# Kernel tuning notes

Measured on AMD Instinct MI355X. Metric: run time of the kernel, lower is better.

## Reference

```python
import jax, jax.numpy as jnp
import numpy as np

B, D, H0, H1, O = 4096, 1024, 1024, 1024, 1024  # O = output_dim + 1
ALPHA = 0.3
CLAMP = 0.3


def setup_inputs() -> dict:
    key = jax.random.key(0)
    ks = jax.random.split(key, 15)
    def he(k, fan_in, shape):
        return jax.random.normal(k, shape, dtype=jnp.float32) * np.sqrt(2.0 / fan_in).astype(np.float32)
    def heb(k, shape):
        return jax.random.uniform(k, shape, dtype=jnp.float32, minval=-CLAMP, maxval=CLAMP)
    return {
        "x": jax.random.normal(ks[0], (B, D), dtype=jnp.float32),
        "x2h0": he(ks[1], D, (D, H0)),
        "x2h1": he(ks[2], D, (D, H1)),
        "h02h1": he(ks[3], H0, (H0, H1)),
        "x2y": he(ks[4], D, (D, O)),
        "h02y": he(ks[5], H0, (H0, O)),
        "h12y": he(ks[6], H1, (H1, O)),
        "heb_x2h0": heb(ks[7], (D, H0)),
        "heb_x2h1": heb(ks[8], (D, H1)),
        "heb_h02h1": heb(ks[9], (H0, H1)),
        "heb_x2y": heb(ks[10], (D, O)),
        "heb_h02y": heb(ks[11], (H0, O)),
        "heb_h12y": heb(ks[12], (H1, O)),
        "W": jax.random.uniform(ks[13], (1, 1), dtype=jnp.float32),
    }


def reference(x, x2h0, x2h1, h02h1, x2y, h02y, h12y,
              heb_x2h0, heb_x2h1, heb_h02h1, heb_x2y, heb_h02y, heb_h12y, W):
    clamp = lambda m: jnp.clip(m, -CLAMP, CLAMP)
    # x -> h0
    h0_x = x @ (x2h0 + W * heb_x2h0)                       # [B, H0]
    heb_x2h0_n = clamp(heb_x2h0 + ALPHA * (x.T @ h0_x))
    h0 = jax.nn.relu(h0_x)
    # x -> h1, h0 -> h1
    h1_x = x @ (x2h1 + W * heb_x2h1)                       # [B, H1]
    heb_x2h1_n = clamp(heb_x2h1 + ALPHA * (x.T @ h1_x))
    h1_0 = h0 @ (h02h1 + W * heb_h02h1)
    heb_h02h1_n = clamp(heb_h02h1 + ALPHA * (h0.T @ h1_0))
    h1 = jax.nn.relu(h1_x + h1_0)
    # x, h0, h1 -> y
    y_x = x @ (x2y + W * heb_x2y)                          # [B, O]
    heb_x2y_n = clamp(heb_x2y + ALPHA * (x.T @ y_x))
    y_0 = h0 @ (h02y + W * heb_h02y)
    heb_h02y_n = clamp(heb_h02y + ALPHA * (h0.T @ y_0))
    y_1 = h1 @ (h12y + W * heb_h12y)
    heb_h12y_n = clamp(heb_h12y + ALPHA * (h1.T @ y_1))
    y = y_x + y_0 + y_1
    W_new = jnp.mean(jnp.tanh(y[:, -2:-1]))               # neuromodulator scalar
    dopa = jnp.mean(jnp.tanh(y[:, -3:-2]))
    y_out = y[:, :-2]                                      # [B, O-2]
    return (y_out, heb_x2h0_n, heb_x2h1_n, heb_h02h1_n,
            heb_x2y_n, heb_h02y_n, heb_h12y_n, W_new, dopa)
```

## Files before the change

### kernel.cpp

```cpp
#include <hip/hip_runtime.h>
#include <stdint.h>

#define ALPHA 0.3f
#define CLAMPV 0.3f
#define BDIM 4096
#define NDIM 1024

typedef float f32x4 __attribute__((ext_vector_type(4)));
typedef __bf16 bf16x8 __attribute__((ext_vector_type(8)));

union U16x8 { uint4 v; unsigned short u[8]; };

__device__ __forceinline__ float bf2f(unsigned short u) {
  union { unsigned int i; float f; } c; c.i = ((unsigned int)u) << 16; return c.f;
}
__device__ __forceinline__ unsigned short f2bf(float f) {
  union { float f; unsigned int i; } c; c.f = f;
  unsigned int u = c.i;
  unsigned int r = u + 0x7FFFu + ((u >> 16) & 1u);
  return (unsigned short)(r >> 16);
}

__global__ __launch_bounds__(256) void fill_k(float* __restrict__ out, int n) {
  int i = blockIdx.x * 256 + threadIdx.x;
  if (i < n) out[i] = 12345.0f;
}

__global__ __launch_bounds__(256) void split_x_k(const float* __restrict__ x,
                                                 unsigned short* __restrict__ hi,
                                                 unsigned short* __restrict__ lo) {
  const size_t i0 = ((size_t)blockIdx.x * 256 + threadIdx.x) * 8;
  f32x4 a = *(const f32x4*)(x + i0);
  f32x4 b = *(const f32x4*)(x + i0 + 4);
  U16x8 h8, l8;
#pragma unroll
  for (int i = 0; i < 4; ++i) {
    unsigned short h = f2bf(a[i]); h8.u[i] = h; l8.u[i] = f2bf(a[i] - bf2f(h));
    unsigned short h2 = f2bf(b[i]); h8.u[4+i] = h2; l8.u[4+i] = f2bf(b[i] - bf2f(h2));
  }
  *(uint4*)(hi + i0) = h8.v;
  *(uint4*)(lo + i0) = l8.v;
}

struct TDesc {
  const void* in1; const void* in2; const float* Wp;
  unsigned short* out_hi; unsigned short* out_lo;
  int R, C, tilesC, mode;
};
struct TBatch { TDesc d[8]; int start[9]; int n; };

__global__ __launch_bounds__(256) void transpose_k(TBatch batch) {
  const int bid = blockIdx.x;
  int g = 0;
#pragma unroll
  for (int i = 1; i < 8; ++i)
    if (i < batch.n && bid >= batch.start[i]) g = i;
  TDesc D = batch.d[g];
  const int lt = bid - batch.start[g];
  const int trow = lt / D.tilesC;
  const int tcol = lt - trow * D.tilesC;
  const int r0 = trow * 64, c0 = tcol * 64;

  __shared__ float tile[64][65];
  const int t = threadIdx.x;
  const int sub = t >> 3, oct = t & 7;
  const float Wv = (D.mode == 2) ? *D.Wp : 0.f;

#pragma unroll
  for (int p = 0; p < 2; ++p) {
    const int rl = p * 32 + sub;
    const int cl0 = oct * 8;
    float vv[8];
    if (D.mode == 0) {
      const unsigned short* ip = (const unsigned short*)D.in1 + (size_t)(r0 + rl) * D.C + c0 + cl0;
      U16x8 tmp; tmp.v = *(const uint4*)ip;
#pragma unroll
      for (int i = 0; i < 8; ++i) vv[i] = bf2f(tmp.u[i]);
    } else {
      const float* ip = (const float*)D.in1 + (size_t)(r0 + rl) * D.C + c0 + cl0;
      f32x4 a = *(const f32x4*)ip, b = *(const f32x4*)(ip + 4);
#pragma unroll
      for (int i = 0; i < 4; ++i) { vv[i] = a[i]; vv[4+i] = b[i]; }
      if (D.mode == 2) {
        const float* ip2 = (const float*)D.in2 + (size_t)(r0 + rl) * D.C + c0 + cl0;
        f32x4 c = *(const f32x4*)ip2, d2 = *(const f32x4*)(ip2 + 4);
#pragma unroll
        for (int i = 0; i < 4; ++i) { vv[i] += Wv * c[i]; vv[4+i] += Wv * d2[i]; }
      }
    }
#pragma unroll
    for (int i = 0; i < 8; ++i) tile[cl0 + i][rl] = vv[i];
  }
  __syncthreads();
#pragma unroll
  for (int p = 0; p < 2; ++p) {
    const int cl = p * 32 + sub;
    const int rl0 = oct * 8;
    U16x8 h8, l8;
#pragma unroll
    for (int i = 0; i < 8; ++i) {
      float v = tile[cl][rl0 + i];
      unsigned short h = f2bf(v);
      h8.u[i] = h;
      l8.u[i] = f2bf(v - bf2f(h));
    }
    const size_t o = (size_t)(c0 + cl) * D.R + r0 + rl0;
    *(uint4*)(D.out_hi + o) = h8.v;
    if (D.mode != 0) *(uint4*)(D.out_lo + o) = l8.v;
  }
}

struct GemmDesc {
  const unsigned short *Ahi, *Alo, *Bhi, *Blo;
  int lda, ldb, nk, accadd;
  float* out32a;
  float* out32b;
  const float* addin;
  unsigned short* sp_hi;
  unsigned short* sp_lo;
  const float* heb_in;
  float* heb_out;
};
struct GemmBatch { GemmDesc d[12]; int start[13]; int n; };

#define AS1 __attribute__((address_space(1)))
#define AS3 __attribute__((address_space(3)))

__global__ __launch_bounds__(256, 2) void gemm_k(GemmBatch batch) {
  const int bid = blockIdx.x;
  int g = 0;
#pragma unroll
  for (int i = 1; i < 12; ++i)
    if (i < batch.n && bid >= batch.start[i]) g = i;
  GemmDesc D = batch.d[g];
  const int local = bid - batch.start[g];
  const int tm = local >> 3;
  const int tn = local & 7;

  __shared__ __align__(16) unsigned short LDS[32768];

  const int t = threadIdx.x;
  const int lane = t & 63;
  const int wave = t >> 6;
  const int wr = wave >> 1, wc = wave & 1;
  const int fr = lane & 15, fg = lane >> 4;

  f32x4 acc[8][4];
#pragma unroll
  for (int i = 0; i < 8; ++i)
#pragma unroll
    for (int j = 0; j < 4; ++j)
#pragma unroll
      for (int r = 0; r < 4; ++r) acc[i][j][r] = 0.f;

  const int r0 = t >> 2;
  const int colSwE = (((t & 3) ^ ((t >> 3) & 3)) << 3);

  size_t aRow[4], bRow[2];
#pragma unroll
  for (int q = 0; q < 4; ++q)
    aRow[q] = (size_t)(tm * 256 + q * 64 + r0) * D.lda + colSwE;
#pragma unroll
  for (int q = 0; q < 2; ++q)
    bRow[q] = (size_t)(tn * 128 + q * 64 + r0) * D.ldb + colSwE;

  const int ldsW = wave * 512;

  auto stageA = [&](const unsigned short* P, int kb, int b) {
    unsigned short* base = LDS + b * 16384 + ldsW;
#pragma unroll
    for (int q = 0; q < 4; ++q)
      __builtin_amdgcn_global_load_lds(
          (const AS1 void*)(P + aRow[q] + kb),
          (AS3 void*)(base + q * 2048), 16, 0, 0);
  };
  auto stageB = [&](const unsigned short* P, int region, int kb, int b) {
    unsigned short* base = LDS + b * 16384 + region + ldsW;
#pragma unroll
    for (int q = 0; q < 2; ++q)
      __builtin_amdgcn_global_load_lds(
          (const AS1 void*)(P + bRow[q] + kb),
          (AS3 void*)(base + q * 2048), 16, 0, 0);
  };

  const int swz = ((fg ^ ((fr >> 1) & 3)) << 4);
  int aoff[8], boff[4];
#pragma unroll
  for (int i = 0; i < 8; ++i)
    aoff[i] = (wr * 128 + i * 16 + fr) * 64 + swz;
#pragma unroll
  for (int j = 0; j < 4; ++j)
    boff[j] = 16384 + (wc * 64 + j * 16 + fr) * 64 + swz;
  const char* ldsc = (const char*)LDS;

  auto computePh0 = [&](int b) {
    const char* bb = ldsc + b * 32768;
    bf16x8 af[8];
#pragma unroll
    for (int i = 0; i < 8; ++i) af[i] = *(const bf16x8*)(bb + aoff[i]);
#pragma unroll
    for (int j = 0; j < 4; ++j) {
      const bf16x8 bh = *(const bf16x8*)(bb + boff[j]);
#pragma unroll
      for (int i = 0; i < 8; ++i)
        acc[i][j] = __builtin_amdgcn_mfma_f32_16x16x32_bf16(af[i], bh, acc[i][j], 0, 0, 0);
      const bf16x8 bl = *(const bf16x8*)(bb + boff[j] + 8192);
#pragma unroll
      for (int i = 0; i < 8; ++i)
        acc[i][j] = __builtin_amdgcn_mfma_f32_16x16x32_bf16(af[i], bl, acc[i][j], 0, 0, 0);
    }
  };
  auto computePh1 = [&](int b) {
    const char* bb = ldsc + b * 32768;
    bf16x8 af[8];
#pragma unroll
    for (int i = 0; i < 8; ++i) af[i] = *(const bf16x8*)(bb + aoff[i]);
#pragma unroll
    for (int j = 0; j < 4; ++j) {
      const bf16x8 bh = *(const bf16x8*)(bb + boff[j]);
#pragma unroll
      for (int i = 0; i < 8; ++i)
        acc[i][j] = __builtin_amdgcn_mfma_f32_16x16x32_bf16(af[i], bh, acc[i][j], 0, 0, 0);
    }
  };

  const int n = D.nk;

  stageA(D.Ahi, 0, 0);
  stageB(D.Bhi, 8192, 0, 0);
  stageB(D.Blo, 12288, 0, 0);
  int buf = 0;

#pragma unroll 1
  for (int kt = 0; kt < n; ++kt) {
    if (kt + 1 < n) {
      const int kb = (kt + 1) << 5;
      stageA(D.Ahi, kb, buf ^ 1);
      stageB(D.Bhi, 8192, kb, buf ^ 1);
      stageB(D.Blo, 12288, kb, buf ^ 1);
      asm volatile("s_waitcnt vmcnt(8)" ::: "memory");
    } else {
      stageA(D.Alo, 0, buf ^ 1);
      stageB(D.Bhi, 8192, 0, buf ^ 1);
      asm volatile("s_waitcnt vmcnt(6)" ::: "memory");
    }
    __builtin_amdgcn_s_barrier();
    __builtin_amdgcn_sched_barrier(0);
    computePh0(buf);
    __builtin_amdgcn_sched_barrier(0);
    __builtin_amdgcn_s_barrier();
    buf ^= 1;
  }

#pragma unroll 1
  for (int kt = 0; kt < n; ++kt) {
    if (kt + 1 < n) {
      const int kb = (kt + 1) << 5;
      stageA(D.Alo, kb, buf ^ 1);
      stageB(D.Bhi, 8192, kb, buf ^ 1);
      asm volatile("s_waitcnt vmcnt(6)" ::: "memory");
    } else {
      asm volatile("s_waitcnt vmcnt(0)" ::: "memory");
    }
    __builtin_amdgcn_s_barrier();
    __builtin_amdgcn_sched_barrier(0);
    computePh1(buf);
    __builtin_amdgcn_sched_barrier(0);
    __builtin_amdgcn_s_barrier();
    buf ^= 1;
  }

  const int grb = tm * 256 + wr * 128 + fg * 4;
  const int gcb = tn * 128 + wc * 64 + fr;
#pragma unroll
  for (int i = 0; i < 8; ++i) {
#pragma unroll
    for (int j = 0; j < 4; ++j) {
      const int gc = gcb + j * 16;
#pragma unroll
      for (int r = 0; r < 4; ++r) {
        const int gr = grb + i * 16 + r;
        const size_t idx = (size_t)gr * NDIM + gc;
        const float v = acc[i][j][r];
        if (D.heb_out) {
          D.heb_out[idx] = fminf(fmaxf(D.heb_in[idx] + ALPHA * v, -CLAMPV), CLAMPV);
        } else {
          if (D.out32a) D.out32a[idx] = v;
          if (D.out32b) D.out32b[idx] = D.accadd ? (D.out32b[idx] + v) : v;
          if (D.sp_hi) {
            float rv = v + (D.addin ? D.addin[idx] : 0.f);
            rv = fmaxf(rv, 0.f);
            const unsigned short h = f2bf(rv);
            D.sp_hi[idx] = h;
            D.sp_lo[idx] = f2bf(rv - bf2f(h));
          }
        }
      }
    }
  }
}

struct HebRed { const float* heb_in; float* out; const float* p[8]; int np; };

__global__ __launch_bounds__(256) void hebred_k(HebRed R) {
  const size_t i0 = ((size_t)blockIdx.x * 256 + threadIdx.x) * 4;
  f32x4 s = *(const f32x4*)(R.p[0] + i0);
#pragma unroll
  for (int k = 1; k < 8; ++k)
    if (k < R.np) s += *(const f32x4*)(R.p[k] + i0);
  f32x4 h = *(const f32x4*)(R.heb_in + i0);
  f32x4 o;
#pragma unroll
  for (int i = 0; i < 4; ++i) o[i] = fminf(fmaxf(h[i] + ALPHA * s[i], -CLAMPV), CLAMPV);
  *(f32x4*)(R.out + i0) = o;
}

__global__ __launch_bounds__(256) void yassm_k(const float* __restrict__ ysum,
                                               float* __restrict__ yout) {
  const int stride = gridDim.x * 256;
  for (int idx = blockIdx.x * 256 + threadIdx.x; idx < BDIM * 1022; idx += stride) {
    const int row = idx / 1022;
    const int col = idx - row * 1022;
    yout[idx] = ysum[(size_t)row * NDIM + col];
  }
}

__global__ __launch_bounds__(256) void tanhcol_k(const float* __restrict__ ysum,
                                                 float* __restrict__ wpart,
                                                 float* __restrict__ dpart) {
  const int r = blockIdx.x * 256 + threadIdx.x;
  const size_t b = (size_t)r * NDIM;
  float tw = tanhf(ysum[b + 1022]);
  float td = tanhf(ysum[b + 1021]);
#pragma unroll
  for (int o = 32; o > 0; o >>= 1) { tw += __shfl_down(tw, o); td += __shfl_down(td, o); }
  __shared__ float s1[4], s2[4];
  const int lane = threadIdx.x & 63, wv = threadIdx.x >> 6;
  if (lane == 0) { s1[wv] = tw; s2[wv] = td; }
  __syncthreads();
  if (threadIdx.x == 0) {
    wpart[blockIdx.x] = s1[0] + s1[1] + s1[2] + s1[3];
    dpart[blockIdx.x] = s2[0] + s2[1] + s2[2] + s2[3];
  }
}

__global__ void finalize_k(const float* __restrict__ wpart, const float* __restrict__ dpart,
                           float* __restrict__ out, int nout) {
  if (threadIdx.x == 0 && blockIdx.x == 0) {
    float s = 0.f, d = 0.f;
    for (int i = 0; i < 16; ++i) { s += wpart[i]; d += dpart[i]; }
    out[nout - 2] = s * (1.f / BDIM);
    out[nout - 1] = d * (1.f / BDIM);
  }
}

extern "C" void kernel_launch(void* const* d_in, const int* in_sizes, int n_in,
                              void* d_out, int out_size, void* d_ws, size_t ws_size,
                              hipStream_t stream) {
  const float* x = (const float*)d_in[0];
  const float* wbase[6]; const float* hebin[6];
  for (int i = 0; i < 6; ++i) { wbase[i] = (const float*)d_in[1 + i]; hebin[i] = (const float*)d_in[7 + i]; }
  const float* Wp = (const float*)d_in[13];
  float* out = (float*)d_out;
  const size_t YOUT = (size_t)BDIM * 1022;
  float* hebout[6];
  for (int i = 0; i < 6; ++i) hebout[i] = out + YOUT + (size_t)i * 1048576;

  const size_t E = (size_t)BDIM * NDIM;
  const size_t PAIRB = E * 4;
  const size_t WPAIRB = (size_t)NDIM * NDIM * 4;
  const size_t FB = E * 4;
  const size_t REQUIRED = 7 * PAIRB + 6 * WPAIRB + 4 * FB;

  if (ws_size < REQUIRED) {
    fill_k<<<(out_size + 255) / 256, 256, 0, stream>>>(out, out_size);
    return;
  }

  char* p = (char*)d_ws;
  auto takeB = [&](size_t n) -> char* { char* q = p; p += n; return q; };

  unsigned short* R0 = (unsigned short*)takeB(PAIRB);
  unsigned short* R1 = (unsigned short*)takeB(PAIRB);
  unsigned short* R2 = (unsigned short*)takeB(PAIRB);
  unsigned short* R3 = (unsigned short*)takeB(PAIRB);
  unsigned short* R4 = (unsigned short*)takeB(PAIRB);
  unsigned short* R5 = (unsigned short*)takeB(PAIRB);
  unsigned short* R6 = (unsigned short*)takeB(PAIRB);
  unsigned short* WThi[6]; unsigned short* WTlo[6];
  for (int i = 0; i < 6; ++i) {
    WThi[i] = (unsigned short*)takeB(WPAIRB);
    WTlo[i] = WThi[i] + (size_t)NDIM * NDIM;
  }
  float* F0 = (float*)takeB(FB);
  float* F1 = (float*)takeB(FB);
  float* F2 = (float*)takeB(FB);
  float* F3 = (float*)takeB(FB);

  unsigned short *xhi = R0, *xlo = R0 + E;
  unsigned short *xThi = R1, *xTlo = R1 + E;
  unsigned short *h0hi = R2, *h0lo = R2 + E;
  unsigned short *h0Thi = R3, *h0Tlo = R3 + E;
  float* part = (float*)R4;
  float* wpart = (float*)R6; float* dpart = wpart + 64;

  split_x_k<<<2048, 256, 0, stream>>>(x, xhi, xlo);

  {
    TBatch tb{};
    int s = 0;
    for (int i = 0; i < 6; ++i) {
      tb.d[i] = { wbase[i], hebin[i], Wp, WThi[i], WTlo[i], NDIM, NDIM, NDIM / 64, 2 };
      tb.start[i] = s; s += (NDIM / 64) * (NDIM / 64);
    }
    tb.d[6] = { x, nullptr, nullptr, xThi, xTlo, BDIM, NDIM, NDIM / 64, 1 };
    tb.start[6] = s; s += (BDIM / 64) * (NDIM / 64);
    tb.start[7] = s; tb.n = 7;
    transpose_k<<<s, 256, 0, stream>>>(tb);
  }

  auto fwdDesc = [&](const unsigned short* ahi, const unsigned short* alo, int wi) -> GemmDesc {
    GemmDesc d{};
    d.Ahi = ahi; d.Alo = alo; d.Bhi = WThi[wi]; d.Blo = WTlo[wi];
    d.lda = NDIM; d.ldb = NDIM; d.nk = NDIM / 32;
    return d;
  };
  auto hebPart = [&](const unsigned short* ahi, const unsigned short* alo,
                     const unsigned short* bhi, const unsigned short* blo,
                     int koff, int klen, float* partOut) -> GemmDesc {
    GemmDesc d{};
    d.Ahi = ahi + koff; d.Alo = alo + koff;
    d.Bhi = bhi + koff; d.Blo = blo + koff;
    d.lda = BDIM; d.ldb = BDIM; d.nk = klen / 32;
    d.out32a = partOut;
    return d;
  };
  auto hebRed = [&](int hi, const float* q0, const float* q1, const float* q2,
                    const float* q3, const float* q4, const float* q5,
                    const float* q6, const float* q7, int np) {
    HebRed r{};
    r.heb_in = hebin[hi]; r.out = hebout[hi];
    r.p[0]=q0; r.p[1]=q1; r.p[2]=q2; r.p[3]=q3; r.p[4]=q4; r.p[5]=q5; r.p[6]=q6; r.p[7]=q7;
    r.np = np;
    hebred_k<<<1024, 256, 0, stream>>>(r);
  };

  {
    GemmBatch gb{};
    gb.d[0] = fwdDesc(xhi, xlo, 0);
    gb.d[0].out32a = F0; gb.d[0].sp_hi = h0hi; gb.d[0].sp_lo = h0lo;
    gb.d[1] = fwdDesc(xhi, xlo, 1);
    gb.d[1].out32a = F1;
    gb.d[2] = fwdDesc(xhi, xlo, 3);
    gb.d[2].out32a = F2; gb.d[2].out32b = F3; gb.d[2].accadd = 0;
    gb.start[0] = 0; gb.start[1] = 128; gb.start[2] = 256; gb.start[3] = 384;
    gb.n = 3;
    gemm_k<<<384, 256, 0, stream>>>(gb);
  }

  {
    TBatch tb{};
    tb.d[0] = { F0, nullptr, nullptr, R4, R4 + E, BDIM, NDIM, NDIM / 64, 1 };
    tb.d[1] = { F1, nullptr, nullptr, R5, R5 + E, BDIM, NDIM, NDIM / 64, 1 };
    tb.d[2] = { F2, nullptr, nullptr, R6, R6 + E, BDIM, NDIM, NDIM / 64, 1 };
    tb.d[3] = { h0hi, nullptr, nullptr, h0Thi, nullptr, BDIM, NDIM, NDIM / 64, 0 };
    tb.d[4] = { h0lo, nullptr, nullptr, h0Tlo, nullptr, BDIM, NDIM, NDIM / 64, 0 };
    for (int i = 0; i < 6; ++i) tb.start[i] = i * 1024;
    tb.n = 5;
    transpose_k<<<5120, 256, 0, stream>>>(tb);
  }

  {
    float* px0a = (float*)WThi[0]; float* px0b = hebout[0];
    float* px1a = (float*)WThi[1]; float* px1b = hebout[1];
    float* pxya = (float*)WThi[3]; float* pxyb = hebout[3];
    GemmBatch gb{};
    gb.d[0] = hebPart(xThi, xTlo, R4, R4 + E, 0,    2048, px0a);
    gb.d[1] = hebPart(xThi, xTlo, R4, R4 + E, 2048, 2048, px0b);
    gb.d[2] = hebPart(xThi, xTlo, R5, R5 + E, 0,    2048, px1a);
    gb.d[3] = hebPart(xThi, xTlo, R5, R5 + E, 2048, 2048, px1b);
    gb.d[4] = hebPart(xThi, xTlo, R6, R6 + E, 0,    2048, pxya);
    gb.d[5] = hebPart(xThi, xTlo, R6, R6 + E, 2048, 2048, pxyb);
    gb.d[6] = fwdDesc(h0hi, h0lo, 2);
    gb.d[6].out32a = F0; gb.d[6].addin = F1; gb.d[6].sp_hi = R0; gb.d[6].sp_lo = R0 + E;
    gb.d[7] = fwdDesc(h0hi, h0lo, 4);
    gb.d[7].out32a = F2; gb.d[7].out32b = F3; gb.d[7].accadd = 1;
    for (int i = 0; i < 6; ++i) gb.start[i] = i * 32;
    gb.start[6] = 192; gb.start[7] = 320; gb.start[8] = 448;
    gb.n = 8;
    gemm_k<<<448, 256, 0, stream>>>(gb);
    hebRed(0, px0a, px0b, 0,0,0,0,0,0, 2);
    hebRed(1, px1a, px1b, 0,0,0,0,0,0, 2);
    hebRed(3, pxya, pxyb, 0,0,0,0,0,0, 2);
  }

  {
    TBatch tb{};
    tb.d[0] = { F0, nullptr, nullptr, R4, R4 + E, BDIM, NDIM, NDIM / 64, 1 };
    tb.d[1] = { F2, nullptr, nullptr, R5, R5 + E, BDIM, NDIM, NDIM / 64, 1 };
    tb.d[2] = { R0, nullptr, nullptr, R1, nullptr, BDIM, NDIM, NDIM / 64, 0 };
    tb.d[3] = { R0 + E, nullptr, nullptr, R1 + E, nullptr, BDIM, NDIM, NDIM / 64, 0 };
    for (int i = 0; i < 5; ++i) tb.start[i] = i * 1024;
    tb.n = 4;
    transpose_k<<<4096, 256, 0, stream>>>(tb);
  }

  {
    float* pa[4] = { (float*)WThi[0], (float*)WThi[1], (float*)WThi[2], (float*)WThi[3] };
    float* pb[4] = { (float*)R6, (float*)R6 + 1048576, (float*)R6 + 2097152, (float*)R6 + 3145728 };
    GemmBatch gb{};
    for (int h = 0; h < 4; ++h) {
      gb.d[h]     = hebPart(h0Thi, h0Tlo, R4, R4 + E, h * 1024, 1024, pa[h]);
      gb.d[4 + h] = hebPart(h0Thi, h0Tlo, R5, R5 + E, h * 1024, 1024, pb[h]);
    }
    gb.d[8] = fwdDesc(R0, R0 + E, 5);
    gb.d[8].out32a = F1; gb.d[8].out32b = F3; gb.d[8].accadd = 1;
    for (int i = 0; i < 8; ++i) gb.start[i] = i * 32;
    gb.start[8] = 256; gb.start[9] = 384;
    gb.n = 9;
    gemm_k<<<384, 256, 0, stream>>>(gb);
    hebRed(2, pa[0], pa[1], pa[2], pa[3], 0,0,0,0, 4);
    hebRed(4, pb[0], pb[1], pb[2], pb[3], 0,0,0,0, 4);
  }

  {
    TBatch tb{};
    tb.d[0] = { F1, nullptr, nullptr, R2, R2 + E, BDIM, NDIM, NDIM / 64, 1 };
    tb.start[0] = 0; tb.start[1] = 1024; tb.n = 1;
    transpose_k<<<1024, 256, 0, stream>>>(tb);
  }

  {
    GemmBatch gb{};
    for (int h = 0; h < 8; ++h)
      gb.d[h] = hebPart(R1, R1 + E, R2, R2 + E, h * 512, 512, part + (size_t)h * 1048576);
    for (int i = 0; i <= 8; ++i) gb.start[i] = i * 32;
    gb.n = 8;
    gemm_k<<<256, 256, 0, stream>>>(gb);
    hebRed(5, part, part + 1048576, part + 2097152, part + 3145728,
           part + 4194304, part + 5242880, part + 6291456, part + 7340032, 8);
  }

  yassm_k<<<2048, 256, 0, stream>>>(F3, out);
  tanhcol_k<<<16, 256, 0, stream>>>(F3, wpart, dpart);
  finalize_k<<<1, 64, 0, stream>>>(wpart, dpart, out, out_size);
}
```

Measured before the change: 513.2 us.

## Remap blocks per XCD, raise MFMA priority, split final heb GEMM 16-way

Block IDs are remapped so that consecutive logical tiles land on the same XCD, which should improve L2 locality for tiles that share A/B panels. s_setprio raises wave priority around the MFMA loops so compute waves are favoured over staging waves. The last heb GEMM (h1.T @ y_1) is split over K into 16 partial GEMMs of length 256 instead of 8 of length 512, which doubles the grid to 512 blocks for better CU occupancy. The cost is a 16-way reduction that reads more partial buffers, and workspace has to be reused across several regions.

```diff
diff --git a/kernel.cpp b/kernel.cpp
--- a/kernel.cpp
+++ b/kernel.cpp
@@ -121,16 +121,20 @@
   const float* heb_in;
   float* heb_out;
 };
-struct GemmBatch { GemmDesc d[12]; int start[13]; int n; };
+struct GemmBatch { GemmDesc d[16]; int start[17]; int n; };
 
 #define AS1 __attribute__((address_space(1)))
 #define AS3 __attribute__((address_space(3)))
 
 __global__ __launch_bounds__(256, 2) void gemm_k(GemmBatch batch) {
-  const int bid = blockIdx.x;
+  const int G = gridDim.x;
+  const int q = G >> 3, r = G & 7;
+  const int xcd = blockIdx.x & 7, idx = blockIdx.x >> 3;
+  const int bid = (xcd < r ? xcd * (q + 1) : r * (q + 1) + (xcd - r) * q) + idx;
+
   int g = 0;
 #pragma unroll
-  for (int i = 1; i < 12; ++i)
+  for (int i = 1; i < 16; ++i)
     if (i < batch.n && bid >= batch.start[i]) g = i;
   GemmDesc D = batch.d[g];
   const int local = bid - batch.start[g];
@@ -151,36 +155,36 @@
 #pragma unroll
     for (int j = 0; j < 4; ++j)
 #pragma unroll
-      for (int r = 0; r < 4; ++r) acc[i][j][r] = 0.f;
+      for (int rr = 0; rr < 4; ++rr) acc[i][j][rr] = 0.f;
 
   const int r0 = t >> 2;
   const int colSwE = (((t & 3) ^ ((t >> 3) & 3)) << 3);
 
   size_t aRow[4], bRow[2];
 #pragma unroll
-  for (int q = 0; q < 4; ++q)
-    aRow[q] = (size_t)(tm * 256 + q * 64 + r0) * D.lda + colSwE;
-#pragma unroll
-  for (int q = 0; q < 2; ++q)
-    bRow[q] = (size_t)(tn * 128 + q * 64 + r0) * D.ldb + colSwE;
+  for (int qq = 0; qq < 4; ++qq)
+    aRow[qq] = (size_t)(tm * 256 + qq * 64 + r0) * D.lda + colSwE;
+#pragma unroll
+  for (int qq = 0; qq < 2; ++qq)
+    bRow[qq] = (size_t)(tn * 128 + qq * 64 + r0) * D.ldb + colSwE;
 
   const int ldsW = wave * 512;
 
   auto stageA = [&](const unsigned short* P, int kb, int b) {
     unsigned short* base = LDS + b * 16384 + ldsW;
 #pragma unroll
-    for (int q = 0; q < 4; ++q)
+    for (int qq = 0; qq < 4; ++qq)
       __builtin_amdgcn_global_load_lds(
-          (const AS1 void*)(P + aRow[q] + kb),
-          (AS3 void*)(base + q * 2048), 16, 0, 0);
+          (const AS1 void*)(P + aRow[qq] + kb),
+          (AS3 void*)(base + qq * 2048), 16, 0, 0);
   };
   auto stageB = [&](const unsigned short* P, int region, int kb, int b) {
     unsigned short* base = LDS + b * 16384 + region + ldsW;
 #pragma unroll
-    for (int q = 0; q < 2; ++q)
+    for (int qq = 0; qq < 2; ++qq)
       __builtin_amdgcn_global_load_lds(
-          (const AS1 void*)(P + bRow[q] + kb),
-          (AS3 void*)(base + q * 2048), 16, 0, 0);
+          (const AS1 void*)(P + bRow[qq] + kb),
+          (AS3 void*)(base + qq * 2048), 16, 0, 0);
   };
 
   const int swz = ((fg ^ ((fr >> 1) & 3)) << 4);
@@ -198,6 +202,7 @@
     bf16x8 af[8];
 #pragma unroll
     for (int i = 0; i < 8; ++i) af[i] = *(const bf16x8*)(bb + aoff[i]);
+    __builtin_amdgcn_s_setprio(1);
 #pragma unroll
     for (int j = 0; j < 4; ++j) {
       const bf16x8 bh = *(const bf16x8*)(bb + boff[j]);
@@ -209,12 +214,14 @@
       for (int i = 0; i < 8; ++i)
         acc[i][j] = __builtin_amdgcn_mfma_f32_16x16x32_bf16(af[i], bl, acc[i][j], 0, 0, 0);
     }
+    __builtin_amdgcn_s_setprio(0);
   };
   auto computePh1 = [&](int b) {
     const char* bb = ldsc + b * 32768;
     bf16x8 af[8];
 #pragma unroll
     for (int i = 0; i < 8; ++i) af[i] = *(const bf16x8*)(bb + aoff[i]);
+    __builtin_amdgcn_s_setprio(1);
 #pragma unroll
     for (int j = 0; j < 4; ++j) {
       const bf16x8 bh = *(const bf16x8*)(bb + boff[j]);
@@ -222,6 +229,7 @@
       for (int i = 0; i < 8; ++i)
         acc[i][j] = __builtin_amdgcn_mfma_f32_16x16x32_bf16(af[i], bh, acc[i][j], 0, 0, 0);
     }
+    __builtin_amdgcn_s_setprio(0);
   };
 
   const int n = D.nk;
@@ -278,10 +286,10 @@
     for (int j = 0; j < 4; ++j) {
       const int gc = gcb + j * 16;
 #pragma unroll
-      for (int r = 0; r < 4; ++r) {
-        const int gr = grb + i * 16 + r;
+      for (int rr = 0; rr < 4; ++rr) {
+        const int gr = grb + i * 16 + rr;
         const size_t idx = (size_t)gr * NDIM + gc;
-        const float v = acc[i][j][r];
+        const float v = acc[i][j][rr];
         if (D.heb_out) {
           D.heb_out[idx] = fminf(fmaxf(D.heb_in[idx] + ALPHA * v, -CLAMPV), CLAMPV);
         } else {
@@ -300,13 +308,13 @@
   }
 }
 
-struct HebRed { const float* heb_in; float* out; const float* p[8]; int np; };
+struct HebRed { const float* heb_in; float* out; const float* p[16]; int np; };
 
 __global__ __launch_bounds__(256) void hebred_k(HebRed R) {
   const size_t i0 = ((size_t)blockIdx.x * 256 + threadIdx.x) * 4;
   f32x4 s = *(const f32x4*)(R.p[0] + i0);
 #pragma unroll
-  for (int k = 1; k < 8; ++k)
+  for (int k = 1; k < 16; ++k)
     if (k < R.np) s += *(const f32x4*)(R.p[k] + i0);
   f32x4 h = *(const f32x4*)(R.heb_in + i0);
   f32x4 o;
@@ -401,8 +409,7 @@
   unsigned short *xThi = R1, *xTlo = R1 + E;
   unsigned short *h0hi = R2, *h0lo = R2 + E;
   unsigned short *h0Thi = R3, *h0Tlo = R3 + E;
-  float* part = (float*)R4;
-  float* wpart = (float*)R6; float* dpart = wpart + 64;
+  float* wpart = (float*)R3; float* dpart = wpart + 64;
 
   split_x_k<<<2048, 256, 0, stream>>>(x, xhi, xlo);
 
@@ -434,15 +441,6 @@
     d.lda = BDIM; d.ldb = BDIM; d.nk = klen / 32;
     d.out32a = partOut;
     return d;
-  };
-  auto hebRed = [&](int hi, const float* q0, const float* q1, const float* q2,
-                    const float* q3, const float* q4, const float* q5,
-                    const float* q6, const float* q7, int np) {
-    HebRed r{};
-    r.heb_in = hebin[hi]; r.out = hebout[hi];
-    r.p[0]=q0; r.p[1]=q1; r.p[2]=q2; r.p[3]=q3; r.p[4]=q4; r.p[5]=q5; r.p[6]=q6; r.p[7]=q7;
-    r.np = np;
-    hebred_k<<<1024, 256, 0, stream>>>(r);
   };
 
   {
@@ -489,9 +487,12 @@
     gb.start[6] = 192; gb.start[7] = 320; gb.start[8] = 448;
     gb.n = 8;
     gemm_k<<<448, 256, 0, stream>>>(gb);
-    hebRed(0, px0a, px0b, 0,0,0,0,0,0, 2);
-    hebRed(1, px1a, px1b, 0,0,0,0,0,0, 2);
-    hebRed(3, pxya, pxyb, 0,0,0,0,0,0, 2);
+    HebRed r0x{}; r0x.heb_in = hebin[0]; r0x.out = hebout[0]; r0x.p[0]=px0a; r0x.p[1]=px0b; r0x.np=2;
+    hebred_k<<<1024, 256, 0, stream>>>(r0x);
+    HebRed r1x{}; r1x.heb_in = hebin[1]; r1x.out = hebout[1]; r1x.p[0]=px1a; r1x.p[1]=px1b; r1x.np=2;
+    hebred_k<<<1024, 256, 0, stream>>>(r1x);
+    HebRed ryx{}; ryx.heb_in = hebin[3]; ryx.out = hebout[3]; ryx.p[0]=pxya; ryx.p[1]=pxyb; ryx.np=2;
+    hebred_k<<<1024, 256, 0, stream>>>(ryx);
   }
 
   {
@@ -519,8 +520,14 @@
     gb.start[8] = 256; gb.start[9] = 384;
     gb.n = 9;
     gemm_k<<<384, 256, 0, stream>>>(gb);
-    hebRed(2, pa[0], pa[1], pa[2], pa[3], 0,0,0,0, 4);
-    hebRed(4, pb[0], pb[1], pb[2], pb[3], 0,0,0,0, 4);
+    HebRed rh{}; rh.heb_in = hebin[2]; rh.out = hebout[2];
+    for (int h = 0; h < 4; ++h) rh.p[h] = pa[h];
+    rh.np = 4;
+    hebred_k<<<1024, 256, 0, stream>>>(rh);
+    HebRed ry{}; ry.heb_in = hebin[4]; ry.out = hebout[4];
+    for (int h = 0; h < 4; ++h) ry.p[h] = pb[h];
+    ry.np = 4;
+    hebred_k<<<1024, 256, 0, stream>>>(ry);
   }
 
   {
@@ -531,14 +538,23 @@
   }
 
   {
+    float* parts[16];
+    for (int h = 0; h < 4; ++h) {
+      parts[h]      = (float*)R4 + (size_t)h * 1048576;
+      parts[4 + h]  = (float*)R5 + (size_t)h * 1048576;
+      parts[8 + h]  = (float*)R6 + (size_t)h * 1048576;
+      parts[12 + h] = (float*)WThi[h];
+    }
     GemmBatch gb{};
-    for (int h = 0; h < 8; ++h)
-      gb.d[h] = hebPart(R1, R1 + E, R2, R2 + E, h * 512, 512, part + (size_t)h * 1048576);
-    for (int i = 0; i <= 8; ++i) gb.start[i] = i * 32;
-    gb.n = 8;
-    gemm_k<<<256, 256, 0, stream>>>(gb);
-    hebRed(5, part, part + 1048576, part + 2097152, part + 3145728,
-           part + 4194304, part + 5242880, part + 6291456, part + 7340032, 8);
+    for (int h = 0; h < 16; ++h)
+      gb.d[h] = hebPart(R1, R1 + E, R2, R2 + E, h * 256, 256, parts[h]);
+    for (int i = 0; i <= 16; ++i) gb.start[i] = i * 32;
+    gb.n = 16;
+    gemm_k<<<512, 256, 0, stream>>>(gb);
+    HebRed rf{}; rf.heb_in = hebin[5]; rf.out = hebout[5];
+    for (int h = 0; h < 16; ++h) rf.p[h] = parts[h];
+    rf.np = 16;
+    hebred_k<<<1024, 256, 0, stream>>>(rf);
   }
 
   yassm_k<<<2048, 256, 0, stream>>>(F3, out);
```

New measurement: 544.0 us. +6.0%, slower.
